# Kernel tuning notes

Measured on AMD Instinct MI355X. Metric: run time of the kernel, lower is better.

Reference implementation:

```python
import jax, jax.numpy as jnp
import numpy as np

ROPE_THETA = 10000.0

def rope(x):
    # RoPE over the FULL model_dim (applied pre head-split, as in the source),
    # interleaved even/odd pairs. x: [B, S, D]
    B, S, D = x.shape
    half = D // 2
    inv_freq = 1.0 / (ROPE_THETA ** (jnp.arange(half, dtype=jnp.float32) * 2.0 / D))
    ang = jnp.arange(S, dtype=jnp.float32)[:, None] * inv_freq[None, :]  # [S, half]
    cos, sin = jnp.cos(ang), jnp.sin(ang)
    x1, x2 = x[..., 0::2], x[..., 1::2]
    r1 = x1 * cos - x2 * sin
    r2 = x1 * sin + x2 * cos
    return jnp.stack([r1, r2], axis=-1).reshape(B, S, D)


def setup_inputs() -> dict:
    key = jax.random.key(0)
    ks = jax.random.split(key, 9)
    B, S, D = 4, 2048, 768
    w = 0.02
    return {
        "X":  jax.random.normal(ks[0], (B, S, D), dtype=jnp.float32),
        "Wq": jax.random.normal(ks[1], (D, D), dtype=jnp.float32) * w,
        "bq": jnp.zeros((D,), dtype=jnp.float32),
        "Wk": jax.random.normal(ks[2], (D, D), dtype=jnp.float32) * w,
        "bk": jnp.zeros((D,), dtype=jnp.float32),
        "Wv": jax.random.normal(ks[3], (D, D), dtype=jnp.float32) * w,
        "bv": jnp.zeros((D,), dtype=jnp.float32),
        "Wo": jax.random.normal(ks[4], (D, D), dtype=jnp.float32) * w,
        "bo": jnp.zeros((D,), dtype=jnp.float32),
    }


def reference(X, Wq, bq, Wk, bk, Wv, bv, Wo, bo):
    NUM_HEADS = 12
    B, S, D = X.shape
    hd = D // NUM_HEADS

    q = rope(X @ Wq + bq)   # RoPE applied pre-split on full model_dim
    k = rope(X @ Wk + bk)
    v = X @ Wv + bv

    # Contiguous per-head slices == reshape to [B, S, H, hd]
    qh = q.reshape(B, S, NUM_HEADS, hd)
    kh = k.reshape(B, S, NUM_HEADS, hd)
    vh = v.reshape(B, S, NUM_HEADS, hd)

    scores = jnp.einsum('bqhd,bkhd->bhqk', qh, kh) / jnp.sqrt(jnp.float32(hd))
    causal = jnp.tril(jnp.ones((S, S), dtype=bool))
    scores = jnp.where(causal[None, None, :, :], scores, -jnp.inf)
    weights = jax.nn.softmax(scores, axis=-1)
    out = jnp.einsum('bhqk,bkhd->bqhd', weights, vh).reshape(B, S, D)
    return out @ Wo + bo
```

## Files before the change

### kernel.cpp

```cpp
#include <hip/hip_runtime.h>
#include <math.h>

#define D_MODEL 768
#define NUM_HEADS 12
#define HEAD_DIM 64
#define SEQ 2048
#define BATCH 4
#define MROWS (BATCH * SEQ)
#define HALF_D (D_MODEL / 2)

typedef __bf16 bf16x8 __attribute__((ext_vector_type(8)));
typedef __bf16 bf16x4 __attribute__((ext_vector_type(4)));
typedef float  f32x4  __attribute__((ext_vector_type(4)));

__device__ __forceinline__ void gload_lds16(const void* gp, void* lp) {
    __builtin_amdgcn_global_load_lds(
        (const __attribute__((address_space(1))) unsigned int*)gp,
        (__attribute__((address_space(3))) unsigned int*)lp, 16, 0, 0);
}

__global__ __launch_bounds__(256)
void rope_table(float2* __restrict__ tab)
{
    int idx = blockIdx.x * 256 + threadIdx.x;
    int s = idx / HALF_D;
    int j = idx - s * HALF_D;
    float freq = __expf(-(float)j * (9.210340371976184f / 384.0f));
    float ang  = (float)s * freq;
    float sn, cs;
    sincosf(ang, &sn, &cs);
    tab[idx] = make_float2(cs, sn);
}

__global__ __launch_bounds__(256)
void cast_x(const float* __restrict__ X, __bf16* __restrict__ Xb)
{
    size_t i = ((size_t)blockIdx.x * 256 + threadIdx.x) * 8;
    float4 u = *(const float4*)(X + i);
    float4 v = *(const float4*)(X + i + 4);
    bf16x8 o;
    o[0]=(__bf16)u.x; o[1]=(__bf16)u.y; o[2]=(__bf16)u.z; o[3]=(__bf16)u.w;
    o[4]=(__bf16)v.x; o[5]=(__bf16)v.y; o[6]=(__bf16)v.z; o[7]=(__bf16)v.w;
    *(bf16x8*)(Xb + i) = o;
}

__global__ __launch_bounds__(256)
void wcast(const float* __restrict__ W0, const float* __restrict__ W1,
           const float* __restrict__ W2, const float* __restrict__ W3,
           __bf16* __restrict__ T0, __bf16* __restrict__ T1,
           __bf16* __restrict__ T2, __bf16* __restrict__ T3)
{
    __shared__ float t[64][65];
    const int z = blockIdx.z;
    const float* W = z == 0 ? W0 : z == 1 ? W1 : z == 2 ? W2 : W3;
    __bf16*      T = z == 0 ? T0 : z == 1 ? T1 : z == 2 ? T2 : T3;

    const int tid = threadIdx.x;
    const int r0 = blockIdx.y * 64, c0 = blockIdx.x * 64;
    const int lx = tid & 63, g = tid >> 6;

    #pragma unroll
    for (int rr = 0; rr < 16; ++rr) {
        int r = g * 16 + rr;
        t[r][lx] = W[(size_t)(r0 + r) * D_MODEL + c0 + lx];
    }
    __syncthreads();

    const int n  = tid >> 2;
    const int kb = (tid & 3) * 16;
    bf16x8 o1, o2;
    #pragma unroll
    for (int m = 0; m < 8; ++m) o1[m] = (__bf16)t[kb + m][n];
    #pragma unroll
    for (int m = 0; m < 8; ++m) o2[m] = (__bf16)t[kb + 8 + m][n];
    __bf16* dst = T + (size_t)(c0 + n) * D_MODEL + r0 + kb;
    *(bf16x8*)dst       = o1;
    *(bf16x8*)(dst + 8) = o2;
}

__global__ __launch_bounds__(256)
void qkv_gemm(const __bf16* __restrict__ Xb,
              const __bf16* __restrict__ Wqt, const __bf16* __restrict__ Wkt,
              const __bf16* __restrict__ Wvt,
              const float* __restrict__ bq, const float* __restrict__ bk,
              const float* __restrict__ bv,
              const float2* __restrict__ tab,
              __bf16* __restrict__ Qb, __bf16* __restrict__ Kb,
              __bf16* __restrict__ Vtb)
{
    __shared__ bf16x8 Asf[8][64];
    __shared__ bf16x8 Bsf[8][64];

    const int tid  = threadIdx.x;
    const int wv   = tid >> 6;
    const int ln   = tid & 63;
    const int t15  = ln & 15;
    const int quad = ln >> 4;
    const int wr = wv >> 1, wc = wv & 1;

    const int which = blockIdx.x / 6;
    const int col0  = (blockIdx.x % 6) * 128;
    const int row0  = blockIdx.y * 128;

    const __bf16* Wt  = which == 0 ? Wqt : which == 1 ? Wkt : Wvt;
    const float* bias = which == 0 ? bq  : which == 1 ? bk  : bv;

    f32x4 acc[4][4];
    #pragma unroll
    for (int i = 0; i < 4; ++i)
        #pragma unroll
        for (int j = 0; j < 4; ++j) acc[i][j] = (f32x4){0.f,0.f,0.f,0.f};

    const __bf16* a0 = Xb + (size_t)(row0 + 16 * wv       + t15) * D_MODEL + 8 * quad;
    const __bf16* a1 = Xb + (size_t)(row0 + 16 * (wv + 4) + t15) * D_MODEL + 8 * quad;
    const __bf16* b0 = Wt + (size_t)(col0 + 16 * wv       + t15) * D_MODEL + 8 * quad;
    const __bf16* b1 = Wt + (size_t)(col0 + 16 * (wv + 4) + t15) * D_MODEL + 8 * quad;

    for (int k0 = 0; k0 < D_MODEL; k0 += 32) {
        __syncthreads();
        gload_lds16(a0 + k0, &Asf[wv][0]);
        gload_lds16(a1 + k0, &Asf[wv + 4][0]);
        gload_lds16(b0 + k0, &Bsf[wv][0]);
        gload_lds16(b1 + k0, &Bsf[wv + 4][0]);
        __syncthreads();

        bf16x8 af[4], bfr[4];
        #pragma unroll
        for (int i = 0; i < 4; ++i) af[i]  = Asf[4 * wr + i][ln];
        #pragma unroll
        for (int j = 0; j < 4; ++j) bfr[j] = Bsf[4 * wc + j][ln];
        #pragma unroll
        for (int i = 0; i < 4; ++i)
            #pragma unroll
            for (int j = 0; j < 4; ++j)
                acc[i][j] = __builtin_amdgcn_mfma_f32_16x16x32_bf16(af[i], bfr[j], acc[i][j], 0, 0, 0);
    }

    #pragma unroll
    for (int i = 0; i < 4; ++i) {
        const int rowb = row0 + 64 * wr + 16 * i + 4 * quad;
        #pragma unroll
        for (int j = 0; j < 4; ++j) {
            const int col = col0 + 64 * wc + 16 * j + t15;
            const float bval = bias[col];
            if (which < 2) {
                const int jh  = col >> 1;
                const float sgn = (col & 1) ? 1.0f : -1.0f;
                const float oscale = (which == 0) ? 0.125f : 1.0f;
                __bf16* dst = (which ? Kb : Qb);
                #pragma unroll
                for (int r = 0; r < 4; ++r) {
                    const int rw = rowb + r;
                    const int s  = rw & (SEQ - 1);
                    float val  = acc[i][j][r] + bval;
                    float part = __shfl_xor(val, 1, 64);
                    float2 cs  = tab[(size_t)s * HALF_D + jh];
                    dst[(size_t)rw * D_MODEL + col] = (__bf16)((val * cs.x + part * sgn * cs.y) * oscale);
                }
            } else {
                const int h = col >> 6, d = col & 63;
                const int bidx = rowb >> 11, s = rowb & (SEQ - 1);
                bf16x4 pk;
                #pragma unroll
                for (int r = 0; r < 4; ++r) pk[r] = (__bf16)(acc[i][j][r] + bval);
                *(bf16x4*)(Vtb + ((size_t)(bidx * NUM_HEADS + h) * 64 + d) * SEQ + s) = pk;
            }
        }
    }
}

__global__ __launch_bounds__(256)
void out_gemm(const __bf16* __restrict__ Ab, const __bf16* __restrict__ Wt,
              const float* __restrict__ bias, float* __restrict__ Cout)
{
    __shared__ bf16x8 Asf[8][64];
    __shared__ bf16x8 Bsf[8][64];

    const int tid  = threadIdx.x;
    const int wv   = tid >> 6;
    const int ln   = tid & 63;
    const int t15  = ln & 15;
    const int quad = ln >> 4;
    const int wr = wv >> 1, wc = wv & 1;

    const int col0 = blockIdx.x * 128;
    const int row0 = blockIdx.y * 128;

    f32x4 acc[4][4];
    #pragma unroll
    for (int i = 0; i < 4; ++i)
        #pragma unroll
        for (int j = 0; j < 4; ++j) acc[i][j] = (f32x4){0.f,0.f,0.f,0.f};

    const __bf16* a0 = Ab + (size_t)(row0 + 16 * wv       + t15) * D_MODEL + 8 * quad;
    const __bf16* a1 = Ab + (size_t)(row0 + 16 * (wv + 4) + t15) * D_MODEL + 8 * quad;
    const __bf16* b0 = Wt + (size_t)(col0 + 16 * wv       + t15) * D_MODEL + 8 * quad;
    const __bf16* b1 = Wt + (size_t)(col0 + 16 * (wv + 4) + t15) * D_MODEL + 8 * quad;

    for (int k0 = 0; k0 < D_MODEL; k0 += 32) {
        __syncthreads();
        gload_lds16(a0 + k0, &Asf[wv][0]);
        gload_lds16(a1 + k0, &Asf[wv + 4][0]);
        gload_lds16(b0 + k0, &Bsf[wv][0]);
        gload_lds16(b1 + k0, &Bsf[wv + 4][0]);
        __syncthreads();

        bf16x8 af[4], bfr[4];
        #pragma unroll
        for (int i = 0; i < 4; ++i) af[i]  = Asf[4 * wr + i][ln];
        #pragma unroll
        for (int j = 0; j < 4; ++j) bfr[j] = Bsf[4 * wc + j][ln];
        #pragma unroll
        for (int i = 0; i < 4; ++i)
            #pragma unroll
            for (int j = 0; j < 4; ++j)
                acc[i][j] = __builtin_amdgcn_mfma_f32_16x16x32_bf16(af[i], bfr[j], acc[i][j], 0, 0, 0);
    }

    #pragma unroll
    for (int i = 0; i < 4; ++i) {
        const int rowb = row0 + 64 * wr + 16 * i + 4 * quad;
        #pragma unroll
        for (int j = 0; j < 4; ++j) {
            const int col = col0 + 64 * wc + 16 * j + t15;
            const float bval = bias[col];
            #pragma unroll
            for (int r = 0; r < 4; ++r)
                Cout[(size_t)(rowb + r) * D_MODEL + col] = acc[i][j][r] + bval;
        }
    }
}

__device__ __forceinline__ void attn_tile(
    const bf16x8 (*Kbuf)[64], const bf16x8 (*Vbuf)[64],
    __bf16 (*Psw)[72],
    bf16x8 aq0, bf16x8 aq1,
    f32x4* o, float* lacc,
    int ln, int t15, int quad, int j0, int qabs, bool domask)
{
    f32x4 s[4];
    #pragma unroll
    for (int c = 0; c < 4; ++c) {
        s[c] = (f32x4){0.f, 0.f, 0.f, 0.f};
        s[c] = __builtin_amdgcn_mfma_f32_16x16x32_bf16(aq0, Kbuf[c][ln],     s[c], 0, 0, 0);
        s[c] = __builtin_amdgcn_mfma_f32_16x16x32_bf16(aq1, Kbuf[4 + c][ln], s[c], 0, 0, 0);
    }

    float p[4][4];
    #pragma unroll
    for (int c = 0; c < 4; ++c)
        #pragma unroll
        for (int r = 0; r < 4; ++r) {
            float e = __expf(s[c][r]);
            if (domask && (j0 + 16 * c + t15 > qabs + r)) e = 0.f;
            p[c][r] = e;
            lacc[r] += e;
        }

    #pragma unroll
    for (int c = 0; c < 4; ++c)
        #pragma unroll
        for (int r = 0; r < 4; ++r)
            Psw[4 * quad + r][16 * c + t15] = (__bf16)p[c][r];
    __asm__ volatile("s_waitcnt lgkmcnt(0)" ::: "memory");

    bf16x8 ap0 = *(const bf16x8*)&Psw[t15][8 * quad];
    bf16x8 ap1 = *(const bf16x8*)&Psw[t15][32 + 8 * quad];

    #pragma unroll
    for (int c = 0; c < 4; ++c) {
        o[c] = __builtin_amdgcn_mfma_f32_16x16x32_bf16(ap0, Vbuf[c][ln],     o[c], 0, 0, 0);
        o[c] = __builtin_amdgcn_mfma_f32_16x16x32_bf16(ap1, Vbuf[4 + c][ln], o[c], 0, 0, 0);
    }
}

__global__ __launch_bounds__(512)
void attn_flash(const __bf16* __restrict__ Q, const __bf16* __restrict__ K,
                const __bf16* __restrict__ Vt, __bf16* __restrict__ O)
{
    __shared__ bf16x8 Kf[2][8][64];
    __shared__ bf16x8 Vf[2][8][64];
    __shared__ __bf16 Psb[8][16][72];

    const int tid  = threadIdx.x;
    const int wv   = tid >> 6;
    const int ln   = tid & 63;
    const int t15  = ln & 15;
    const int quad = ln >> 4;

    const int n  = blockIdx.x;
    const int sb = n >> 8;
    const int tb = n & 255;
    const int a  = tb & 15;
    const int qt = (sb == 0) ? a : (sb == 1) ? (15 - a) : ((a + 8) & 15);
    const int bh = (tb >> 4) + 16 * sb;
    const int b  = bh / NUM_HEADS;
    const int h  = bh % NUM_HEADS;
    const int q0 = qt * 128;
    const int nt = (q0 >> 6) + 2;

    bf16x8 aq0, aq1;
    {
        const __bf16* qs = Q + (size_t)(b * SEQ + q0 + 16 * wv + t15) * D_MODEL + h * 64 + 8 * quad;
        aq0 = *(const bf16x8*)qs;
        aq1 = *(const bf16x8*)(qs + 32);
    }

    const __bf16* kp = K  + ((size_t)b * SEQ + 16 * (wv & 3) + t15) * D_MODEL
                          + h * 64 + 32 * (wv >> 2) + 8 * quad;
    const __bf16* vp = Vt + ((size_t)bh * 64 + 16 * (wv & 3) + t15) * SEQ
                          + 32 * (wv >> 2) + 8 * quad;

    f32x4 o[4];
    #pragma unroll
    for (int c = 0; c < 4; ++c) o[c] = (f32x4){0.f,0.f,0.f,0.f};
    float lacc[4] = {0.f, 0.f, 0.f, 0.f};
    const int qabs = q0 + 16 * wv + 4 * quad;

    gload_lds16(kp, &Kf[0][wv][0]);
    gload_lds16(vp, &Vf[0][wv][0]);

    int cur = 0;
    for (int it = 0; it < nt; ++it) {
        __syncthreads();
        if (it + 1 < nt) {
            const int jn = (it + 1) * 64;
            gload_lds16(kp + (size_t)jn * D_MODEL, &Kf[cur ^ 1][wv][0]);
            gload_lds16(vp + jn,                   &Vf[cur ^ 1][wv][0]);
        }
        const int j0 = it * 64;
        const bool domask = (j0 + 63) > (q0 + 16 * wv);
        attn_tile(Kf[cur], Vf[cur], Psb[wv], aq0, aq1, o, lacc,
                  ln, t15, quad, j0, qabs, domask);
        cur ^= 1;
    }

    #pragma unroll
    for (int off = 1; off < 16; off <<= 1)
        #pragma unroll
        for (int r = 0; r < 4; ++r)
            lacc[r] += __shfl_xor(lacc[r], off, 64);

    float inv[4];
    #pragma unroll
    for (int r = 0; r < 4; ++r) inv[r] = 1.0f / lacc[r];
    #pragma unroll
    for (int c = 0; c < 4; ++c)
        #pragma unroll
        for (int r = 0; r < 4; ++r) {
            int row = qabs + r;
            O[(size_t)(b * SEQ + row) * D_MODEL + h * 64 + 16 * c + t15] = (__bf16)(o[c][r] * inv[r]);
        }
}

extern "C" void kernel_launch(void* const* d_in, const int* in_sizes, int n_in,
                              void* d_out, int out_size, void* d_ws, size_t ws_size,
                              hipStream_t stream) {
    const float* X  = (const float*)d_in[0];
    const float* Wq = (const float*)d_in[1];
    const float* bq = (const float*)d_in[2];
    const float* Wk = (const float*)d_in[3];
    const float* bk = (const float*)d_in[4];
    const float* Wv = (const float*)d_in[5];
    const float* bv = (const float*)d_in[6];
    const float* Wo = (const float*)d_in[7];
    const float* bo = (const float*)d_in[8];
    float* out = (float*)d_out;

    const size_t BSD = (size_t)MROWS * D_MODEL;
    const size_t WSZ = (size_t)D_MODEL * D_MODEL;

    __bf16* Xb  = (__bf16*)d_ws;
    __bf16* Qb  = Xb  + BSD;
    __bf16* Kb  = Qb  + BSD;
    __bf16* Vtb = Kb  + BSD;
    __bf16* Ob  = Vtb + BSD;
    __bf16* Wqt = Ob  + BSD;
    __bf16* Wkt = Wqt + WSZ;
    __bf16* Wvt = Wkt + WSZ;
    __bf16* Wot = Wvt + WSZ;
    float2* Tab = (float2*)(Wot + WSZ);

    rope_table<<<(SEQ * HALF_D) / 256, 256, 0, stream>>>(Tab);
    cast_x<<<BSD / (256 * 8), 256, 0, stream>>>(X, Xb);
    wcast<<<dim3(12, 12, 4), 256, 0, stream>>>(Wq, Wk, Wv, Wo, Wqt, Wkt, Wvt, Wot);

    qkv_gemm<<<dim3(18, 64), 256, 0, stream>>>(Xb, Wqt, Wkt, Wvt, bq, bk, bv, Tab, Qb, Kb, Vtb);

    attn_flash<<<768, 512, 0, stream>>>(Qb, Kb, Vtb, Ob);

    out_gemm<<<dim3(6, 64), 256, 0, stream>>>(Ob, Wot, bo, out);
}
```

Before: 269.0 us.

## Replace LDS-staged GEMM loops with register double-buffered direct global loads

Both the QKV and output projection GEMMs stop staging tiles through shared memory with two barriers per k-step. Each wave now loads its MFMA fragments straight from global memory into registers and prefetches the next k-slice while computing the current one. The output GEMM also switches to 64x128 tiles, which doubles the grid to give more blocks. This removes barrier and LDS round-trip overhead, at the cost of redundant global loads across waves that must now be served by L1/L2, and higher register pressure.

New measurement: 358.5 us. +33.3%, slower.

```diff
diff --git a/kernel.cpp b/kernel.cpp
--- a/kernel.cpp
+++ b/kernel.cpp
@@ -88,9 +88,6 @@
               __bf16* __restrict__ Qb, __bf16* __restrict__ Kb,
               __bf16* __restrict__ Vtb)
 {
-    __shared__ bf16x8 Asf[8][64];
-    __shared__ bf16x8 Bsf[8][64];
-
     const int tid  = threadIdx.x;
     const int wv   = tid >> 6;
     const int ln   = tid & 63;
@@ -105,35 +102,38 @@
     const __bf16* Wt  = which == 0 ? Wqt : which == 1 ? Wkt : Wvt;
     const float* bias = which == 0 ? bq  : which == 1 ? bk  : bv;
 
+    const __bf16* Abase = Xb + (size_t)(row0 + 64 * wr + t15) * D_MODEL + 8 * quad;
+    const __bf16* Bbase = Wt + (size_t)(col0 + 64 * wc + t15) * D_MODEL + 8 * quad;
+
     f32x4 acc[4][4];
     #pragma unroll
     for (int i = 0; i < 4; ++i)
         #pragma unroll
         for (int j = 0; j < 4; ++j) acc[i][j] = (f32x4){0.f,0.f,0.f,0.f};
 
-    const __bf16* a0 = Xb + (size_t)(row0 + 16 * wv       + t15) * D_MODEL + 8 * quad;
-    const __bf16* a1 = Xb + (size_t)(row0 + 16 * (wv + 4) + t15) * D_MODEL + 8 * quad;
-    const __bf16* b0 = Wt + (size_t)(col0 + 16 * wv       + t15) * D_MODEL + 8 * quad;
-    const __bf16* b1 = Wt + (size_t)(col0 + 16 * (wv + 4) + t15) * D_MODEL + 8 * quad;
-
-    for (int k0 = 0; k0 < D_MODEL; k0 += 32) {
-        __syncthreads();
-        gload_lds16(a0 + k0, &Asf[wv][0]);
-        gload_lds16(a1 + k0, &Asf[wv + 4][0]);
-        gload_lds16(b0 + k0, &Bsf[wv][0]);
-        gload_lds16(b1 + k0, &Bsf[wv + 4][0]);
-        __syncthreads();
-
-        bf16x8 af[4], bfr[4];
-        #pragma unroll
-        for (int i = 0; i < 4; ++i) af[i]  = Asf[4 * wr + i][ln];
-        #pragma unroll
-        for (int j = 0; j < 4; ++j) bfr[j] = Bsf[4 * wc + j][ln];
+    bf16x8 af[2][4], bfr[2][4];
+    #pragma unroll
+    for (int i = 0; i < 4; ++i) {
+        af[0][i]  = *(const bf16x8*)(Abase + (size_t)(16 * i) * D_MODEL);
+        bfr[0][i] = *(const bf16x8*)(Bbase + (size_t)(16 * i) * D_MODEL);
+    }
+
+    #pragma unroll
+    for (int s = 0; s < 24; ++s) {
+        const int cur = s & 1, nxt = cur ^ 1;
+        if (s + 1 < 24) {
+            const int kn = (s + 1) * 32;
+            #pragma unroll
+            for (int i = 0; i < 4; ++i) {
+                af[nxt][i]  = *(const bf16x8*)(Abase + (size_t)(16 * i) * D_MODEL + kn);
+                bfr[nxt][i] = *(const bf16x8*)(Bbase + (size_t)(16 * i) * D_MODEL + kn);
+            }
+        }
         #pragma unroll
         for (int i = 0; i < 4; ++i)
             #pragma unroll
             for (int j = 0; j < 4; ++j)
-                acc[i][j] = __builtin_amdgcn_mfma_f32_16x16x32_bf16(af[i], bfr[j], acc[i][j], 0, 0, 0);
+                acc[i][j] = __builtin_amdgcn_mfma_f32_16x16x32_bf16(af[cur][i], bfr[cur][j], acc[i][j], 0, 0, 0);
     }
 
     #pragma unroll
@@ -173,56 +173,57 @@
 void out_gemm(const __bf16* __restrict__ Ab, const __bf16* __restrict__ Wt,
               const float* __restrict__ bias, float* __restrict__ Cout)
 {
-    __shared__ bf16x8 Asf[8][64];
-    __shared__ bf16x8 Bsf[8][64];
-
     const int tid  = threadIdx.x;
     const int wv   = tid >> 6;
     const int ln   = tid & 63;
     const int t15  = ln & 15;
     const int quad = ln >> 4;
-    const int wr = wv >> 1, wc = wv & 1;
 
     const int col0 = blockIdx.x * 128;
-    const int row0 = blockIdx.y * 128;
-
-    f32x4 acc[4][4];
+    const int row0 = blockIdx.y * 64;
+
+    const __bf16* Abase = Ab + (size_t)(row0 + t15) * D_MODEL + 8 * quad;
+    const __bf16* Bbase = Wt + (size_t)(col0 + 32 * wv + t15) * D_MODEL + 8 * quad;
+
+    f32x4 acc[4][2];
     #pragma unroll
     for (int i = 0; i < 4; ++i)
         #pragma unroll
-        for (int j = 0; j < 4; ++j) acc[i][j] = (f32x4){0.f,0.f,0.f,0.f};
-
-    const __bf16* a0 = Ab + (size_t)(row0 + 16 * wv       + t15) * D_MODEL + 8 * quad;
-    const __bf16* a1 = Ab + (size_t)(row0 + 16 * (wv + 4) + t15) * D_MODEL + 8 * quad;
-    const __bf16* b0 = Wt + (size_t)(col0 + 16 * wv       + t15) * D_MODEL + 8 * quad;
-    const __bf16* b1 = Wt + (size_t)(col0 + 16 * (wv + 4) + t15) * D_MODEL + 8 * quad;
-
-    for (int k0 = 0; k0 < D_MODEL; k0 += 32) {
-        __syncthreads();
-        gload_lds16(a0 + k0, &Asf[wv][0]);
-        gload_lds16(a1 + k0, &Asf[wv + 4][0]);
-        gload_lds16(b0 + k0, &Bsf[wv][0]);
-        gload_lds16(b1 + k0, &Bsf[wv + 4][0]);
-        __syncthreads();
-
-        bf16x8 af[4], bfr[4];
-        #pragma unroll
-        for (int i = 0; i < 4; ++i) af[i]  = Asf[4 * wr + i][ln];
-        #pragma unroll
-        for (int j = 0; j < 4; ++j) bfr[j] = Bsf[4 * wc + j][ln];
+        for (int j = 0; j < 2; ++j) acc[i][j] = (f32x4){0.f,0.f,0.f,0.f};
+
+    bf16x8 af[2][4], bfr[2][2];
+    #pragma unroll
+    for (int i = 0; i < 4; ++i)
+        af[0][i]  = *(const bf16x8*)(Abase + (size_t)(16 * i) * D_MODEL);
+    #pragma unroll
+    for (int j = 0; j < 2; ++j)
+        bfr[0][j] = *(const bf16x8*)(Bbase + (size_t)(16 * j) * D_MODEL);
+
+    #pragma unroll
+    for (int s = 0; s < 24; ++s) {
+        const int cur = s & 1, nxt = cur ^ 1;
+        if (s + 1 < 24) {
+            const int kn = (s + 1) * 32;
+            #pragma unroll
+            for (int i = 0; i < 4; ++i)
+                af[nxt][i]  = *(const bf16x8*)(Abase + (size_t)(16 * i) * D_MODEL + kn);
+            #pragma unroll
+            for (int j = 0; j < 2; ++j)
+                bfr[nxt][j] = *(const bf16x8*)(Bbase + (size_t)(16 * j) * D_MODEL + kn);
+        }
         #pragma unroll
         for (int i = 0; i < 4; ++i)
             #pragma unroll
-            for (int j = 0; j < 4; ++j)
-                acc[i][j] = __builtin_amdgcn_mfma_f32_16x16x32_bf16(af[i], bfr[j], acc[i][j], 0, 0, 0);
+            for (int j = 0; j < 2; ++j)
+                acc[i][j] = __builtin_amdgcn_mfma_f32_16x16x32_bf16(af[cur][i], bfr[cur][j], acc[i][j], 0, 0, 0);
     }
 
     #pragma unroll
     for (int i = 0; i < 4; ++i) {
-        const int rowb = row0 + 64 * wr + 16 * i + 4 * quad;
-        #pragma unroll
-        for (int j = 0; j < 4; ++j) {
-            const int col = col0 + 64 * wc + 16 * j + t15;
+        const int rowb = row0 + 16 * i + 4 * quad;
+        #pragma unroll
+        for (int j = 0; j < 2; ++j) {
+            const int col = col0 + 32 * wv + 16 * j + t15;
             const float bval = bias[col];
             #pragma unroll
             for (int r = 0; r < 4; ++r)
@@ -389,5 +390,5 @@
 
     attn_flash<<<768, 512, 0, stream>>>(Qb, Kb, Vtb, Ob);
 
-    out_gemm<<<dim3(6, 64), 256, 0, stream>>>(Ob, Wot, bo, out);
-}
+    out_gemm<<<dim3(6, 128), 256, 0, stream>>>(Ob, Wot, bo, out);
+}
```
